# Optimization experiments

Measured on AMD Instinct MI355X. Metric: run time of the kernel, lower is better.

The kernel has to match this reference:

```python
import jax, jax.numpy as jnp
import numpy as np

N_NODES = 100000
N_EDGES = 1600000
IN_DIM = 128
OUT_DIM = 32
N_HEADS = 4
NEG_SLOPE = 0.2  # DGL GATConv default LeakyReLU negative slope


def setup_inputs() -> dict:
    key = jax.random.key(0)
    k_h, k_src, k_dst, k_w, k_al, k_ar = jax.random.split(key, 6)
    h = jax.random.normal(k_h, (N_NODES, IN_DIM), dtype=jnp.float32)
    src = jax.random.randint(k_src, (N_EDGES,), 0, N_NODES, dtype=jnp.int32)
    dst = jnp.sort(jax.random.randint(k_dst, (N_EDGES,), 0, N_NODES, dtype=jnp.int32))
    # Xavier-ish init scale
    W = jax.random.normal(k_w, (IN_DIM, N_HEADS * OUT_DIM), dtype=jnp.float32) / np.sqrt(IN_DIM)
    attn_l = jax.random.normal(k_al, (N_HEADS, OUT_DIM), dtype=jnp.float32) / np.sqrt(OUT_DIM)
    attn_r = jax.random.normal(k_ar, (N_HEADS, OUT_DIM), dtype=jnp.float32) / np.sqrt(OUT_DIM)
    bias = jnp.zeros((N_HEADS * OUT_DIM,), dtype=jnp.float32)
    return {"h": h, "src": src, "dst": dst, "W": W, "attn_l": attn_l, "attn_r": attn_r, "bias": bias}


def reference(h, src, dst, W, attn_l, attn_r, bias):
    # Eval-mode GATConv (feat_drop / attn_drop disabled).
    N = h.shape[0]
    # Linear projection -> [N, H, D]
    feat = (h @ W).reshape(N, N_HEADS, OUT_DIM)
    # Per-node attention logits: el/er [N, H]
    el = jnp.einsum('nhd,hd->nh', feat, attn_l)
    er = jnp.einsum('nhd,hd->nh', feat, attn_r)
    # Edge scores: e = LeakyReLU(el[src] + er[dst])  -> [E, H]
    e = el[src] + er[dst]
    e = jnp.where(e > 0, e, NEG_SLOPE * e)
    # Segment softmax over incoming edges of each destination node
    e_max = jax.ops.segment_max(e, dst, num_segments=N, indices_are_sorted=True)
    e_exp = jnp.exp(e - e_max[dst])
    denom = jax.ops.segment_sum(e_exp, dst, num_segments=N, indices_are_sorted=True)
    alpha = e_exp / denom[dst]  # [E, H]
    # Weighted aggregate: sum_e alpha[e] * feat[src[e]] per destination
    msg = feat[src] * alpha[:, :, None]  # [E, H, D]
    rst = jax.ops.segment_sum(msg, dst, num_segments=N, indices_are_sorted=True)  # [N, H, D]
    # Bias + ReLU activation (GATLayer default activation=F.relu)
    rst = rst + bias.reshape(1, N_HEADS, OUT_DIM)
    return jax.nn.relu(rst)
```

## Files before the change

### kernel.cpp

```cpp
#include <hip/hip_runtime.h>
#include <hip/hip_fp16.h>
#include <math.h>

#define NEG_SLOPE 0.2f

typedef _Float16 f16x2 __attribute__((ext_vector_type(2)));
typedef _Float16 f16x8 __attribute__((ext_vector_type(8)));
typedef float f32x4 __attribute__((ext_vector_type(4)));

__device__ __forceinline__ float fdot2f(unsigned int a, unsigned int b, float c) {
#if __has_builtin(__builtin_amdgcn_fdot2)
    return __builtin_amdgcn_fdot2(__builtin_bit_cast(f16x2, a),
                                  __builtin_bit_cast(f16x2, b), c, false);
#else
    __half2 ah = __builtin_bit_cast(__half2, a), bh = __builtin_bit_cast(__half2, b);
    float2 af = __half22float2(ah), bf = __half22float2(bh);
    return c + af.x * bf.x + af.y * bf.y;
#endif
}

__device__ __forceinline__ unsigned int packw(float a, float b) {
#if __has_builtin(__builtin_amdgcn_cvt_pkrtz)
    return __builtin_bit_cast(unsigned int, __builtin_amdgcn_cvt_pkrtz(a, b));
#else
    return __builtin_bit_cast(unsigned int, __floats2half2_rn(a, b));
#endif
}

__global__ __launch_bounds__(256) void prep_seg_kernel(
    const float* __restrict__ W, __half* __restrict__ w16t,
    const float* __restrict__ attn_l, const float* __restrict__ attn_r,
    __half* __restrict__ al16, __half* __restrict__ ar16,
    const int* __restrict__ dst, int* __restrict__ off, int E, int N)
{
    const int b = blockIdx.x;
    if (b < 64) {
        int tid = b * 256 + threadIdx.x;
        int c = tid >> 7, k = tid & 127;
        w16t[c * 128 + k] = __float2half(W[k * 128 + c]);
        if (tid < 128) {
            al16[tid] = __float2half(attn_l[tid]);
            ar16[tid] = __float2half(attn_r[tid]);
        }
        return;
    }
    int i = (b - 64) * 256 + threadIdx.x;
    if (i >= E) return;
    int d = dst[i];
    int prev = (i == 0) ? -1 : dst[i - 1];
    for (int n = prev + 1; n <= d; ++n) off[n] = i;
    if (i == E - 1) {
        for (int n = d + 1; n <= N; ++n) off[n] = E;
    }
}

__global__ __launch_bounds__(512) void proj_kernel(
    const float* __restrict__ h, const __half* __restrict__ w16t,
    const __half* __restrict__ al16, const __half* __restrict__ ar16,
    __half* __restrict__ feat, float* __restrict__ el, float* __restrict__ er,
    int N)
{
    __shared__ __half hl[128 * 128];
    __shared__ __half wl[128 * 128];
    const int t = threadIdx.x;
    const int nodeBase = blockIdx.x * 128;

#pragma unroll
    for (int i = 0; i < 4; ++i) {
        int ch = t + i * 512;
        int col = ch >> 4, k8 = ch & 15;
        uint4 v = *(const uint4*)(w16t + col * 128 + k8 * 8);
        int byte = col * 256 + k8 * 16;
        *(uint4*)((char*)wl + (byte ^ ((col & 7) << 4))) = v;
    }
#pragma unroll
    for (int i = 0; i < 8; ++i) {
        int slot = t + i * 512;
        int row = slot >> 5, c4 = slot & 31;
        int gn = nodeBase + row;
        float4 v = make_float4(0.f, 0.f, 0.f, 0.f);
        if (gn < N) v = *(const float4*)(h + (size_t)gn * 128 + c4 * 4);
        __half2 p0 = __floats2half2_rn(v.x, v.y);
        __half2 p1 = __floats2half2_rn(v.z, v.w);
        uint2 u = make_uint2(__builtin_bit_cast(unsigned int, p0),
                             __builtin_bit_cast(unsigned int, p1));
        int byte = row * 256 + c4 * 8;
        *(uint2*)((char*)hl + (byte ^ ((row & 7) << 4))) = u;
    }
    __syncthreads();

    const int l = t & 63, wave = t >> 6;
    const int arow = wave * 16 + (l & 15);
    const int kg = l >> 4;
    f32x4 acc[8];
#pragma unroll
    for (int i = 0; i < 8; ++i) acc[i] = (f32x4){0.f, 0.f, 0.f, 0.f};

#pragma unroll
    for (int kt = 0; kt < 4; ++kt) {
        const int kb = (kt * 32 + kg * 8) * 2;
        f16x8 a = *(const f16x8*)((const char*)hl +
                    ((arow * 256 + kb) ^ ((arow & 7) << 4)));
#pragma unroll
        for (int ct = 0; ct < 8; ++ct) {
            int bcol = ct * 16 + (l & 15);
            f16x8 b = *(const f16x8*)((const char*)wl +
                        ((bcol * 256 + kb) ^ ((bcol & 7) << 4)));
            acc[ct] = __builtin_amdgcn_mfma_f32_16x16x32_f16(a, b, acc[ct], 0, 0, 0);
        }
    }

    __syncthreads();
    const int colLo = l & 15;
    const int rowHi = wave * 16 + (l >> 4) * 4;
#pragma unroll
    for (int ct = 0; ct < 8; ++ct) {
#pragma unroll
        for (int r = 0; r < 4; ++r) {
            int row = rowHi + r;
            int byte = row * 256 + (ct * 16 + colLo) * 2;
            *(__half*)((char*)hl + (byte ^ ((row & 7) << 4))) = __float2half(acc[ct][r]);
        }
    }
    __syncthreads();

    {
        const int row = t >> 2, head = t & 3;
        const int node = nodeBase + row;
        float lv = 0.f, rv = 0.f;
#pragma unroll
        for (int j = 0; j < 4; ++j) {
            int byte = row * 256 + head * 64 + j * 16;
            uint4 f = *(const uint4*)((const char*)hl + (byte ^ ((row & 7) << 4)));
            uint4 a = *(const uint4*)(al16 + head * 32 + j * 8);
            uint4 bb = *(const uint4*)(ar16 + head * 32 + j * 8);
            lv = fdot2f(f.x, a.x, lv); rv = fdot2f(f.x, bb.x, rv);
            lv = fdot2f(f.y, a.y, lv); rv = fdot2f(f.y, bb.y, rv);
            lv = fdot2f(f.z, a.z, lv); rv = fdot2f(f.z, bb.z, rv);
            lv = fdot2f(f.w, a.w, lv); rv = fdot2f(f.w, bb.w, rv);
        }
        if (node < N) {
            el[(size_t)node * 4 + head] = lv;
            er[(size_t)node * 4 + head] = rv;
        }
    }

    char* featB = (char*)feat + (size_t)nodeBase * 256;
#pragma unroll
    for (int i = 0; i < 4; ++i) {
        int c = t + i * 512;
        int row = c >> 4;
        uint4 v = *(const uint4*)((const char*)hl + ((c * 16) ^ ((row & 7) << 4)));
        if (nodeBase + row < N) *(uint4*)(featB + c * 16) = v;
    }
}

__global__ __launch_bounds__(256) void aggregate_kernel(
    const __half* __restrict__ feat, const float* __restrict__ el,
    const float* __restrict__ er, const int* __restrict__ off,
    const int* __restrict__ src, const float* __restrict__ bias,
    float* __restrict__ out, int N)
{
    const int wid = (int)((blockIdx.x * blockDim.x + threadIdx.x) >> 6);
    const int l = threadIdx.x & 63;
    if (wid >= N) return;
    const int n = __builtin_amdgcn_readfirstlane(wid);
    const int s = off[n];
    const int e = off[n + 1];
    const int f0 = 2 * l;
    const int hm = l >> 4;
    const float b0 = bias[f0], b1 = bias[f0 + 1];
    float* outp = out + (size_t)n * 128;
    if (s >= e) {
        outp[f0] = fmaxf(b0, 0.f);
        outp[f0 + 1] = fmaxf(b1, 0.f);
        return;
    }

    const float er_mine = er[n * 4 + hm];
    const float er_coop = er[n * 4 + (l & 3)];
    float ax = 0.f, ay = 0.f, dn = 0.f;
    const unsigned int one2 = 0x3C003C00u;

    int ei = s;
    for (; ei + 16 <= e; ei += 16) {
        int sv[16];
#pragma unroll
        for (int k = 0; k < 16; ++k) sv[k] = src[ei + k];
        int svc = src[ei + (l >> 2)];
        float sc = el[(size_t)svc * 4 + (l & 3)] + er_coop;
        sc = sc > 0.f ? sc : NEG_SLOPE * sc;
        float myw = __expf(sc);
        unsigned int g[16];
#pragma unroll
        for (int k = 0; k < 16; ++k)
            g[k] = *(const unsigned int*)(feat + (size_t)sv[k] * 128 + f0);
#pragma unroll
        for (int k = 0; k < 8; ++k) {
            float wa = __shfl(myw, 8 * k + hm);
            float wb = __shfl(myw, 8 * k + 4 + hm);
            unsigned int w2 = packw(wa, wb);
            unsigned int lo = __builtin_amdgcn_perm(g[2 * k + 1], g[2 * k], 0x05040100u);
            unsigned int hi = __builtin_amdgcn_perm(g[2 * k + 1], g[2 * k], 0x07060302u);
            ax = fdot2f(w2, lo, ax);
            ay = fdot2f(w2, hi, ay);
            dn = fdot2f(w2, one2, dn);
        }
    }
    if (ei + 8 <= e) {
        int sv[8];
#pragma unroll
        for (int k = 0; k < 8; ++k) sv[k] = src[ei + k];
        int svc = src[ei + ((l >> 2) & 7)];
        float sc = el[(size_t)svc * 4 + (l & 3)] + er_coop;
        sc = sc > 0.f ? sc : NEG_SLOPE * sc;
        float myw = __expf(sc);
        unsigned int g[8];
#pragma unroll
        for (int k = 0; k < 8; ++k)
            g[k] = *(const unsigned int*)(feat + (size_t)sv[k] * 128 + f0);
#pragma unroll
        for (int k = 0; k < 4; ++k) {
            float wa = __shfl(myw, 8 * k + hm);
            float wb = __shfl(myw, 8 * k + 4 + hm);
            unsigned int w2 = packw(wa, wb);
            unsigned int lo = __builtin_amdgcn_perm(g[2 * k + 1], g[2 * k], 0x05040100u);
            unsigned int hi = __builtin_amdgcn_perm(g[2 * k + 1], g[2 * k], 0x07060302u);
            ax = fdot2f(w2, lo, ax);
            ay = fdot2f(w2, hi, ay);
            dn = fdot2f(w2, one2, dn);
        }
        ei += 8;
    }
    if (ei + 4 <= e) {
        int sv0 = src[ei], sv1 = src[ei + 1], sv2 = src[ei + 2], sv3 = src[ei + 3];
        float e0 = el[(size_t)sv0 * 4 + hm], e1 = el[(size_t)sv1 * 4 + hm];
        float e2 = el[(size_t)sv2 * 4 + hm], e3 = el[(size_t)sv3 * 4 + hm];
        unsigned int g0 = *(const unsigned int*)(feat + (size_t)sv0 * 128 + f0);
        unsigned int g1 = *(const unsigned int*)(feat + (size_t)sv1 * 128 + f0);
        unsigned int g2 = *(const unsigned int*)(feat + (size_t)sv2 * 128 + f0);
        unsigned int g3 = *(const unsigned int*)(feat + (size_t)sv3 * 128 + f0);
        float s0 = e0 + er_mine, s1 = e1 + er_mine, s2 = e2 + er_mine, s3 = e3 + er_mine;
        s0 = s0 > 0.f ? s0 : NEG_SLOPE * s0;
        s1 = s1 > 0.f ? s1 : NEG_SLOPE * s1;
        s2 = s2 > 0.f ? s2 : NEG_SLOPE * s2;
        s3 = s3 > 0.f ? s3 : NEG_SLOPE * s3;
        unsigned int w2a = packw(__expf(s0), __expf(s1));
        unsigned int w2b = packw(__expf(s2), __expf(s3));
        unsigned int lo = __builtin_amdgcn_perm(g1, g0, 0x05040100u);
        unsigned int hi = __builtin_amdgcn_perm(g1, g0, 0x07060302u);
        ax = fdot2f(w2a, lo, ax); ay = fdot2f(w2a, hi, ay); dn = fdot2f(w2a, one2, dn);
        lo = __builtin_amdgcn_perm(g3, g2, 0x05040100u);
        hi = __builtin_amdgcn_perm(g3, g2, 0x07060302u);
        ax = fdot2f(w2b, lo, ax); ay = fdot2f(w2b, hi, ay); dn = fdot2f(w2b, one2, dn);
        ei += 4;
    }
    for (; ei < e; ++ei) {
        int sv = src[ei];
        float sc = el[(size_t)sv * 4 + hm] + er_mine;
        sc = sc > 0.f ? sc : NEG_SLOPE * sc;
        float w = __expf(sc);
        __half2 gh = *(const __half2*)(feat + (size_t)sv * 128 + f0);
        float2 fv = __half22float2(gh);
        ax += w * fv.x; ay += w * fv.y; dn += w;
    }
    const float inv = 1.f / dn;
    *(float2*)(outp + f0) = make_float2(fmaxf(ax * inv + b0, 0.f),
                                        fmaxf(ay * inv + b1, 0.f));
}

extern "C" void kernel_launch(void* const* d_in, const int* in_sizes, int n_in,
                              void* d_out, int out_size, void* d_ws, size_t ws_size,
                              hipStream_t stream)
{
    const float* h      = (const float*)d_in[0];
    const int*   src    = (const int*)d_in[1];
    const int*   dst    = (const int*)d_in[2];
    const float* W      = (const float*)d_in[3];
    const float* attn_l = (const float*)d_in[4];
    const float* attn_r = (const float*)d_in[5];
    const float* bias   = (const float*)d_in[6];
    const int N = in_sizes[0] / 128;
    const int E = in_sizes[1];
    float* out = (float*)d_out;

    char* ws = (char*)d_ws;
    __half* feat = (__half*)ws;            ws += (size_t)N * 128 * sizeof(__half);
    float*  el   = (float*)ws;             ws += (size_t)N * 4 * sizeof(float);
    float*  er   = (float*)ws;             ws += (size_t)N * 4 * sizeof(float);
    __half* w16t = (__half*)ws;            ws += 128 * 128 * sizeof(__half);
    __half* al16 = (__half*)ws;            ws += 256;
    __half* ar16 = (__half*)ws;            ws += 256;
    int*    off  = (int*)ws;

    hipLaunchKernelGGL(prep_seg_kernel, dim3(64 + (E + 255) / 256), dim3(256), 0, stream,
                       W, w16t, attn_l, attn_r, al16, ar16, dst, off, E, N);
    hipLaunchKernelGGL(proj_kernel, dim3((N + 127) / 128), dim3(512), 0, stream,
                       h, w16t, al16, ar16, feat, el, er, N);
    hipLaunchKernelGGL(aggregate_kernel, dim3((N + 3) / 4), dim3(256), 0, stream,
                       feat, el, er, off, src, bias, out, N);
}
```

Before: 103.3 us.

## Quantize features to int8 per node and precompute edge weights in separate pass

The projection kernel now stores node features as 8-bit offset-quantized values with a per-node scale instead of fp16, halving the gathered bytes per edge. A new edge kernel precomputes the exp attention weights and the scale-multiplied weights per head in head-major fp16 arrays. The aggregation then reads these contiguously and dequantizes via an fp16 exponent-bias trick, subtracting the offset term at the end. This adds an extra pass over the edges that writes and rereads 16 bytes per edge, and int8 quantization lowers accuracy.

```diff
diff --git a/kernel.cpp b/kernel.cpp
--- a/kernel.cpp
+++ b/kernel.cpp
@@ -19,14 +19,6 @@
 #endif
 }
 
-__device__ __forceinline__ unsigned int packw(float a, float b) {
-#if __has_builtin(__builtin_amdgcn_cvt_pkrtz)
-    return __builtin_bit_cast(unsigned int, __builtin_amdgcn_cvt_pkrtz(a, b));
-#else
-    return __builtin_bit_cast(unsigned int, __floats2half2_rn(a, b));
-#endif
-}
-
 __global__ __launch_bounds__(256) void prep_seg_kernel(
     const float* __restrict__ W, __half* __restrict__ w16t,
     const float* __restrict__ attn_l, const float* __restrict__ attn_r,
@@ -57,8 +49,8 @@
 __global__ __launch_bounds__(512) void proj_kernel(
     const float* __restrict__ h, const __half* __restrict__ w16t,
     const __half* __restrict__ al16, const __half* __restrict__ ar16,
-    __half* __restrict__ feat, float* __restrict__ el, float* __restrict__ er,
-    int N)
+    unsigned char* __restrict__ feat8, float* __restrict__ scale,
+    float* __restrict__ el, float* __restrict__ er, int N)
 {
     __shared__ __half hl[128 * 128];
     __shared__ __half wl[128 * 128];
@@ -145,27 +137,91 @@
         }
     }
 
-    char* featB = (char*)feat + (size_t)nodeBase * 256;
-#pragma unroll
-    for (int i = 0; i < 4; ++i) {
-        int c = t + i * 512;
-        int row = c >> 4;
-        uint4 v = *(const uint4*)((const char*)hl + ((c * 16) ^ ((row & 7) << 4)));
-        if (nodeBase + row < N) *(uint4*)(featB + c * 16) = v;
-    }
+    {
+        const int r = t >> 2, q = t & 3;
+        uint4 c4[4];
+#pragma unroll
+        for (int j = 0; j < 4; ++j) {
+            int ch = r * 16 + q * 4 + j;
+            c4[j] = *(const uint4*)((const char*)hl + ((ch * 16) ^ ((r & 7) << 4)));
+        }
+        float mx = 1e-20f;
+#pragma unroll
+        for (int j = 0; j < 4; ++j) {
+            const __half2* hp = (const __half2*)&c4[j];
+#pragma unroll
+            for (int u = 0; u < 4; ++u) {
+                float2 f = __half22float2(hp[u]);
+                mx = fmaxf(mx, fmaxf(fabsf(f.x), fabsf(f.y)));
+            }
+        }
+        mx = fmaxf(mx, __shfl_xor(mx, 1));
+        mx = fmaxf(mx, __shfl_xor(mx, 2));
+        const float qinv = 127.f / mx;
+        const int node = nodeBase + r;
+        if (q == 0 && node < N) scale[node] = mx * (1.f / 127.f);
+        unsigned int outw[8];
+#pragma unroll
+        for (int j = 0; j < 4; ++j) {
+            const __half2* hp = (const __half2*)&c4[j];
+#pragma unroll
+            for (int u = 0; u < 2; ++u) {
+                float2 fa = __half22float2(hp[2 * u]);
+                float2 fb = __half22float2(hp[2 * u + 1]);
+                unsigned i0 = (unsigned)(__float2int_rn(fa.x * qinv) + 128) & 255;
+                unsigned i1 = (unsigned)(__float2int_rn(fa.y * qinv) + 128) & 255;
+                unsigned i2 = (unsigned)(__float2int_rn(fb.x * qinv) + 128) & 255;
+                unsigned i3 = (unsigned)(__float2int_rn(fb.y * qinv) + 128) & 255;
+                outw[j * 2 + u] = i0 | (i1 << 8) | (i2 << 16) | (i3 << 24);
+            }
+        }
+        if (node < N) {
+            uint4* d4 = (uint4*)(feat8 + (size_t)node * 128 + q * 32);
+            d4[0] = make_uint4(outw[0], outw[1], outw[2], outw[3]);
+            d4[1] = make_uint4(outw[4], outw[5], outw[6], outw[7]);
+        }
+    }
+}
+
+__global__ __launch_bounds__(256) void edgew_kernel(
+    const float* __restrict__ el, const float* __restrict__ er,
+    const float* __restrict__ scale, const int* __restrict__ src,
+    const int* __restrict__ dst, __half* __restrict__ w_t,
+    __half* __restrict__ ws_t, int E)
+{
+    int e = blockIdx.x * 256 + threadIdx.x;
+    if (e >= E) return;
+    int sv = src[e], dv = dst[e];
+    float4 a = *(const float4*)(el + (size_t)sv * 4);
+    float4 b = *(const float4*)(er + (size_t)dv * 4);
+    float scl = scale[sv];
+    float s0 = a.x + b.x, s1 = a.y + b.y, s2 = a.z + b.z, s3 = a.w + b.w;
+    s0 = s0 > 0.f ? s0 : NEG_SLOPE * s0;
+    s1 = s1 > 0.f ? s1 : NEG_SLOPE * s1;
+    s2 = s2 > 0.f ? s2 : NEG_SLOPE * s2;
+    s3 = s3 > 0.f ? s3 : NEG_SLOPE * s3;
+    float w0 = __expf(s0), w1 = __expf(s1), w2 = __expf(s2), w3 = __expf(s3);
+    w_t[e]                  = __float2half(w0);
+    w_t[(size_t)E + e]      = __float2half(w1);
+    w_t[(size_t)2 * E + e]  = __float2half(w2);
+    w_t[(size_t)3 * E + e]  = __float2half(w3);
+    ws_t[e]                 = __float2half(w0 * scl);
+    ws_t[(size_t)E + e]     = __float2half(w1 * scl);
+    ws_t[(size_t)2 * E + e] = __float2half(w2 * scl);
+    ws_t[(size_t)3 * E + e] = __float2half(w3 * scl);
 }
 
 __global__ __launch_bounds__(256) void aggregate_kernel(
-    const __half* __restrict__ feat, const float* __restrict__ el,
-    const float* __restrict__ er, const int* __restrict__ off,
+    const unsigned char* __restrict__ feat8, const __half* __restrict__ w_t,
+    const __half* __restrict__ ws_t, const int* __restrict__ off,
     const int* __restrict__ src, const float* __restrict__ bias,
-    float* __restrict__ out, int N)
+    float* __restrict__ out, int N, int E)
 {
     const int wid = (int)((blockIdx.x * blockDim.x + threadIdx.x) >> 6);
     const int l = threadIdx.x & 63;
     if (wid >= N) return;
     const int n = __builtin_amdgcn_readfirstlane(wid);
-    const int s = off[n];
+    int s = off[n];
     const int e = off[n + 1];
     const int f0 = 2 * l;
     const int hm = l >> 4;
@@ -177,96 +233,108 @@
         return;
     }
 
-    const float er_mine = er[n * 4 + hm];
-    const float er_coop = er[n * 4 + (l & 3)];
-    float ax = 0.f, ay = 0.f, dn = 0.f;
+    const __half* wp  = w_t  + (size_t)hm * E;
+    const __half* wsp = ws_t + (size_t)hm * E;
+    float ax = 0.f, ay = 0.f, dn = 0.f, dnw = 0.f;
     const unsigned int one2 = 0x3C003C00u;
+    const unsigned int bias2 = 0x66006600u;
+
+    if (s & 1) {
+        unsigned int gg = *(const unsigned short*)(feat8 + (size_t)src[s] * 128 + f0);
+        float w  = __half2float(wp[s]);
+        float wsv = __half2float(wsp[s]);
+        ax += wsv * (float)(1536 + (gg & 0xFF));
+        ay += wsv * (float)(1536 + (gg >> 8));
+        dn += w; dnw += wsv;
+        ++s;
+    }
 
     int ei = s;
     for (; ei + 16 <= e; ei += 16) {
         int sv[16];
 #pragma unroll
         for (int k = 0; k < 16; ++k) sv[k] = src[ei + k];
-        int svc = src[ei + (l >> 2)];
-        float sc = el[(size_t)svc * 4 + (l & 3)] + er_coop;
-        sc = sc > 0.f ? sc : NEG_SLOPE * sc;
-        float myw = __expf(sc);
+        unsigned int w2[8], ws2[8];
+#pragma unroll
+        for (int k = 0; k < 8; ++k) {
+            w2[k]  = *(const unsigned int*)(wp + ei + 2 * k);
+            ws2[k] = *(const unsigned int*)(wsp + ei + 2 * k);
+        }
         unsigned int g[16];
 #pragma unroll
         for (int k = 0; k < 16; ++k)
-            g[k] = *(const unsigned int*)(feat + (size_t)sv[k] * 128 + f0);
+            g[k] = *(const unsigned short*)(feat8 + (size_t)sv[k] * 128 + f0);
 #pragma unroll
         for (int k = 0; k < 8; ++k) {
-            float wa = __shfl(myw, 8 * k + hm);
-            float wb = __shfl(myw, 8 * k + 4 + hm);
-            unsigned int w2 = packw(wa, wb);
-            unsigned int lo = __builtin_amdgcn_perm(g[2 * k + 1], g[2 * k], 0x05040100u);
-            unsigned int hi = __builtin_amdgcn_perm(g[2 * k + 1], g[2 * k], 0x07060302u);
-            ax = fdot2f(w2, lo, ax);
-            ay = fdot2f(w2, hi, ay);
-            dn = fdot2f(w2, one2, dn);
+            unsigned int comb = g[2 * k] | (g[2 * k + 1] << 16);
+            unsigned int ux = (comb & 0x00FF00FFu) | bias2;
+            unsigned int uy = ((comb >> 8) & 0x00FF00FFu) | bias2;
+            ax  = fdot2f(ws2[k], ux, ax);
+            ay  = fdot2f(ws2[k], uy, ay);
+            dn  = fdot2f(w2[k], one2, dn);
+            dnw = fdot2f(ws2[k], one2, dnw);
         }
     }
     if (ei + 8 <= e) {
         int sv[8];
 #pragma unroll
         for (int k = 0; k < 8; ++k) sv[k] = src[ei + k];
-        int svc = src[ei + ((l >> 2) & 7)];
-        float sc = el[(size_t)svc * 4 + (l & 3)] + er_coop;
-        sc = sc > 0.f ? sc : NEG_SLOPE * sc;
-        float myw = __expf(sc);
+        unsigned int w2[4], ws2[4];
+#pragma unroll
+        for (int k = 0; k < 4; ++k) {
+            w2[k]  = *(const unsigned int*)(wp + ei + 2 * k);
+            ws2[k] = *(const unsigned int*)(wsp + ei + 2 * k);
+        }
         unsigned int g[8];
 #pragma unroll
         for (int k = 0; k < 8; ++k)
-            g[k] = *(const unsigned int*)(feat + (size_t)sv[k] * 128 + f0);
+            g[k] = *(const unsigned short*)(feat8 + (size_t)sv[k] * 128 + f0);
 #pragma unroll
         for (int k = 0; k < 4; ++k) {
-            float wa = __shfl(myw, 8 * k + hm);
-            float wb = __shfl(myw, 8 * k + 4 + hm);
-            unsigned int w2 = packw(wa, wb);
-            unsigned int lo = __builtin_amdgcn_perm(g[2 * k + 1], g[2 * k], 0x05040100u);
-            unsigned int hi = __builtin_amdgcn_perm(g[2 * k + 1], g[2 * k], 0x07060302u);
-            ax = fdot2f(w2, lo, ax);
-            ay = fdot2f(w2, hi, ay);
-            dn = fdot2f(w2, one2, dn);
+            unsigned int comb = g[2 * k] | (g[2 * k + 1] << 16);
+            unsigned int ux = (comb & 0x00FF00FFu) | bias2;
+            unsigned int uy = ((comb >> 8) & 0x00FF00FFu) | bias2;
+            ax  = fdot2f(ws2[k], ux, ax);
+            ay  = fdot2f(ws2[k], uy, ay);
+            dn  = fdot2f(w2[k], one2, dn);
+            dnw = fdot2f(ws2[k], one2, dnw);
         }
         ei += 8;
     }
     if (ei + 4 <= e) {
-        int sv0 = src[ei], sv1 = src[ei + 1], sv2 = src[ei + 2], sv3 = src[ei + 3];
-        float e0 = el[(size_t)sv0 * 4 + hm], e1 = el[(size_t)sv1 * 4 + hm];
-        float e2 = el[(size_t)sv2 * 4 + hm], e3 = el[(size_t)sv3 * 4 + hm];
-        unsigned int g0 = *(const unsigned int*)(feat + (size_t)sv0 * 128 + f0);
-        unsigned int g1 = *(const unsigned int*)(feat + (size_t)sv1 * 128 + f0);
-        unsigned int g2 = *(const unsigned int*)(feat + (size_t)sv2 * 128 + f0);
-        unsigned int g3 = *(const unsigned int*)(feat + (size_t)sv3 * 128 + f0);
-        float s0 = e0 + er_mine, s1 = e1 + er_mine, s2 = e2 + er_mine, s3 = e3 + er_mine;
-        s0 = s0 > 0.f ? s0 : NEG_SLOPE * s0;
-        s1 = s1 > 0.f ? s1 : NEG_SLOPE * s1;
-        s2 = s2 > 0.f ? s2 : NEG_SLOPE * s2;
-        s3 = s3 > 0.f ? s3 : NEG_SLOPE * s3;
-        unsigned int w2a = packw(__expf(s0), __expf(s1));
-        unsigned int w2b = packw(__expf(s2), __expf(s3));
-        unsigned int lo = __builtin_amdgcn_perm(g1, g0, 0x05040100u);
-        unsigned int hi = __builtin_amdgcn_perm(g1, g0, 0x07060302u);
-        ax = fdot2f(w2a, lo, ax); ay = fdot2f(w2a, hi, ay); dn = fdot2f(w2a, one2, dn);
-        lo = __builtin_amdgcn_perm(g3, g2, 0x05040100u);
-        hi = __builtin_amdgcn_perm(g3, g2, 0x07060302u);
-        ax = fdot2f(w2b, lo, ax); ay = fdot2f(w2b, hi, ay); dn = fdot2f(w2b, one2, dn);
+        int sv0 = src[ei], sv1 = src[ei + 1], sv2_ = src[ei + 2], sv3 = src[ei + 3];
+        unsigned int w2a  = *(const unsigned int*)(wp + ei);
+        unsigned int w2b  = *(const unsigned int*)(wp + ei + 2);
+        unsigned int ws2a = *(const unsigned int*)(wsp + ei);
+        unsigned int ws2b = *(const unsigned int*)(wsp + ei + 2);
+        unsigned int g0 = *(const unsigned short*)(feat8 + (size_t)sv0 * 128 + f0);
+        unsigned int g1 = *(const unsigned short*)(feat8 + (size_t)sv1 * 128 + f0);
+        unsigned int g2 = *(const unsigned short*)(feat8 + (size_t)sv2_ * 128 + f0);
+        unsigned int g3 = *(const unsigned short*)(feat8 + (size_t)sv3 * 128 + f0);
+        unsigned int comb = g0 | (g1 << 16);
+        unsigned int ux = (comb & 0x00FF00FFu) | bias2;
+        unsigned int uy = ((comb >> 8) & 0x00FF00FFu) | bias2;
+        ax = fdot2f(ws2a, ux, ax); ay = fdot2f(ws2a, uy, ay);
+        dn = fdot2f(w2a, one2, dn); dnw = fdot2f(ws2a, one2, dnw);
+        comb = g2 | (g3 << 16);
+        ux = (comb & 0x00FF00FFu) | bias2;
+        uy = ((comb >> 8) & 0x00FF00FFu) | bias2;
+        ax = fdot2f(ws2b, ux, ax); ay = fdot2f(ws2b, uy, ay);
+        dn = fdot2f(w2b, one2, dn); dnw = fdot2f(ws2b, one2, dnw);
         ei += 4;
     }
     for (; ei < e; ++ei) {
-        int sv = src[ei];
-        float sc = el[(size_t)sv * 4 + hm] + er_mine;
-        sc = sc > 0.f ? sc : NEG_SLOPE * sc;
-        float w = __expf(sc);
-        __half2 gh = *(const __half2*)(feat + (size_t)sv * 128 + f0);
-        float2 fv = __half22float2(gh);
-        ax += w * fv.x; ay += w * fv.y; dn += w;
+        unsigned int gg = *(const unsigned short*)(feat8 + (size_t)src[ei] * 128 + f0);
+        float w  = __half2float(wp[ei]);
+        float wsv = __half2float(wsp[ei]);
+        ax += wsv * (float)(1536 + (gg & 0xFF));
+        ay += wsv * (float)(1536 + (gg >> 8));
+        dn += w; dnw += wsv;
     }
     const float inv = 1.f / dn;
-    *(float2*)(outp + f0) = make_float2(fmaxf(ax * inv + b0, 0.f),
-                                        fmaxf(ay * inv + b1, 0.f));
+    const float rx = (ax - 1664.f * dnw) * inv + b0;
+    const float ry = (ay - 1664.f * dnw) * inv + b1;
+    *(float2*)(outp + f0) = make_float2(fmaxf(rx, 0.f), fmaxf(ry, 0.f));
 }
 
 extern "C" void kernel_launch(void* const* d_in, const int* in_sizes, int n_in,
@@ -285,18 +353,23 @@
     float* out = (float*)d_out;
 
     char* ws = (char*)d_ws;
-    __half* feat = (__half*)ws;            ws += (size_t)N * 128 * sizeof(__half);
-    float*  el   = (float*)ws;             ws += (size_t)N * 4 * sizeof(float);
-    float*  er   = (float*)ws;             ws += (size_t)N * 4 * sizeof(float);
-    __half* w16t = (__half*)ws;            ws += 128 * 128 * sizeof(__half);
-    __half* al16 = (__half*)ws;            ws += 256;
-    __half* ar16 = (__half*)ws;            ws += 256;
-    int*    off  = (int*)ws;
+    unsigned char* feat8 = (unsigned char*)ws; ws += (size_t)N * 128;
+    float*  scale = (float*)ws;            ws += (size_t)N * sizeof(float);
+    float*  el    = (float*)ws;            ws += (size_t)N * 4 * sizeof(float);
+    float*  er    = (float*)ws;            ws += (size_t)N * 4 * sizeof(float);
+    __half* w_t   = (__half*)ws;           ws += (size_t)E * 4 * sizeof(__half);
+    __half* ws_t  = (__half*)ws;           ws += (size_t)E * 4 * sizeof(__half);
+    __half* w16t  = (__half*)ws;           ws += 128 * 128 * sizeof(__half);
+    __half* al16  = (__half*)ws;           ws += 256;
+    __half* ar16  = (__half*)ws;           ws += 256;
+    int*    off   = (int*)ws;
 
     hipLaunchKernelGGL(prep_seg_kernel, dim3(64 + (E + 255) / 256), dim3(256), 0, stream,
                        W, w16t, attn_l, attn_r, al16, ar16, dst, off, E, N);
     hipLaunchKernelGGL(proj_kernel, dim3((N + 127) / 128), dim3(512), 0, stream,
-                       h, w16t, al16, ar16, feat, el, er, N);
+                       h, w16t, al16, ar16, feat8, scale, el, er, N);
+    hipLaunchKernelGGL(edgew_kernel, dim3((E + 255) / 256), dim3(256), 0, stream,
+                       el, er, scale, src, dst, w_t, ws_t, E);
     hipLaunchKernelGGL(aggregate_kernel, dim3((N + 3) / 4), dim3(256), 0, stream,
-                       feat, el, er, off, src, bias, out, N);
-}
+                       feat8, w_t, ws_t, off, src, bias, out, N, E);
+}
```

New measurement: 114.4 us. +10.7%, slower.
